# Optimization experiments

Hardware: AMD Instinct MI355X
Metric: run time of the kernel (lower is better)

Reference implementation:

```python
import jax, jax.numpy as jnp
import numpy as np

B, S, F, H, E = 32, 2048, 16, 64, 256

def setup_inputs() -> dict:
    key = jax.random.key(0)
    ks = jax.random.split(key, 7)
    x = jax.random.normal(ks[0], (B, S, F), dtype=jnp.float32)
    masked_index = jax.random.randint(ks[1], (B, S, F), 0, 2) > 0
    W1 = jax.random.normal(ks[2], (F, H), dtype=jnp.float32) * 0.1
    b1 = jax.random.normal(ks[3], (F, H), dtype=jnp.float32) * 0.1
    W2 = jax.random.normal(ks[4], (F, E, H), dtype=jnp.float32) * 0.1
    b2 = jax.random.normal(ks[5], (F, E), dtype=jnp.float32) * 0.1
    masked_values = jax.random.normal(ks[6], (F, E), dtype=jnp.float32)
    return {"x": x, "masked_index": masked_index, "W1": W1, "b1": b1,
            "W2": W2, "b2": b2, "masked_values": masked_values}

def reference(x, masked_index, W1, b1, W2, b2, masked_values):
    # Per-feature 1->64 linear: x[...,None] * W1[f] + b1[f]  -> [B,S,F,H]
    h = jax.nn.gelu(x[..., None] * W1 + b1, approximate=False)
    # dropout is identity in eval mode
    # Per-feature 64->E linear (batched over F): [B,S,F,E]
    embeds = jnp.einsum('bsfh,feh->bsfe', h, W2) + b2
    # Replace masked positions with learned masked_values, then sum over features
    embeds = jnp.where(masked_index[..., None], masked_values, embeds)
    return jnp.sum(embeds, axis=-2)  # [B,S,E]
```

## Files before the change

### kernel.cpp

```cpp
#include <hip/hip_runtime.h>
#include <hip/hip_bf16.h>
#include <cstdint>
#include <math.h>


#define F_ 16
#define H_ 64
#define E_ 256
#define BM 128
#define NT 512
#define BS_TOTAL 65536
#define XSCALE 6.0f

typedef __attribute__((ext_vector_type(8))) short s16x8;
typedef __attribute__((ext_vector_type(4))) float f32x4;

__device__ __forceinline__ unsigned short f2bf(float f){
  unsigned u = __builtin_bit_cast(unsigned, f);
  u += 0x7FFFu + ((u >> 16) & 1u);
  return (unsigned short)(u >> 16);
}
__device__ __forceinline__ unsigned cvtpk(float a, float b){
  unsigned r; asm("v_cvt_pk_bf16_f32 %0, %1, %2" : "=v"(r) : "v"(a), "v"(b)); return r;
}

__global__ __launch_bounds__(256)
void prep_cmat(const float* __restrict__ W1, const float* __restrict__ b1,
               const float* __restrict__ W2, const float* __restrict__ b2,
               const float* __restrict__ mv, unsigned short* __restrict__ Cmat){
  const int f = blockIdx.x, t = threadIdx.x;
  __shared__ float hs[16][H_];
  __shared__ float ct[14][16];

  #pragma unroll
  for (int s = 0; s < 4; ++s){
    int idx = t + s * 256;
    int j = idx >> 6, h = idx & 63;
    float xj = XSCALE * cosf(3.14159265358979f * (j + 0.5f) / 16.0f);
    float z = xj * W1[f * H_ + h] + b1[f * H_ + h];
    hs[j][h] = 0.5f * z * (1.0f + erff(z * 0.7071067811865475f));
  }
  if (t < 224){
    int d = t >> 4, j = t & 15;
    ct[d][j] = cosf(3.14159265358979f * (d + 1) * (j + 0.5f) / 16.0f) * 0.125f;
  }
  __syncthreads();

  const int e = t;
  const float4* w2p = (const float4*)(W2 + ((long)f * E_ + e) * H_);
  float b2v = b2[f * E_ + e];
  float ph[16];
  #pragma unroll
  for (int j = 0; j < 16; ++j) ph[j] = b2v;
  #pragma unroll
  for (int hq = 0; hq < 16; ++hq){
    float4 w = w2p[hq];
    #pragma unroll
    for (int j = 0; j < 16; ++j){
      const float4 hv = *(const float4*)&hs[j][hq * 4];
      ph[j] += w.x * hv.x + w.y * hv.y + w.z * hv.z + w.w * hv.w;
    }
  }
  float s0 = 0.f;
  #pragma unroll
  for (int j = 0; j < 16; ++j) s0 += ph[j];
  float c0 = s0 * 0.0625f;

  float vals[16];
  #pragma unroll
  for (int d = 0; d < 14; ++d){
    float c = 0.f;
    #pragma unroll
    for (int j = 0; j < 16; ++j) c += ph[j] * ct[d][j];
    vals[d] = c;
  }
  vals[14] = mv[f * E_ + e] - c0;
  vals[15] = c0;

  const int lane = (f >> 2) * 16 + (e & 15);
  const int eb = e >> 4;
  #pragma unroll
  for (int g = 0; g < 2; ++g){
    int kk = g * 4 + (f & 3);
    unsigned w[4];
    w[0] = (unsigned)f2bf(vals[g*8+0]) | ((unsigned)f2bf(vals[g*8+1]) << 16);
    w[1] = (unsigned)f2bf(vals[g*8+2]) | ((unsigned)f2bf(vals[g*8+3]) << 16);
    w[2] = (unsigned)f2bf(vals[g*8+4]) | ((unsigned)f2bf(vals[g*8+5]) << 16);
    w[3] = (unsigned)f2bf(vals[g*8+6]) | ((unsigned)f2bf(vals[g*8+7]) << 16);
    long byte = ((long)(kk * 16 + eb) * 64 + lane) * 16;
    *(uint4*)((char*)Cmat + byte) = *(uint4*)w;
  }
}

__global__ __launch_bounds__(NT)
void ts_main(const float* __restrict__ x, const int* __restrict__ mask,
             const unsigned short* __restrict__ Cmat, float* __restrict__ out){
  const int tid = threadIdx.x, lane = tid & 63, wid = tid >> 6;
  const int wm = wid >> 2, wn = wid & 3;
  const int rr = lane & 15;
  const int q  = lane >> 4;
  const int rowBase = blockIdx.x * BM;

  int rows[4];
  #pragma unroll
  for (int m = 0; m < 4; ++m) rows[m] = rowBase + wm * 64 + m * 16 + rr;

  float4 x4[4]; int4 mk4[4];
  #pragma unroll
  for (int m = 0; m < 4; ++m){
    x4[m]  = *(const float4*)&x[rows[m] * F_ + q * 4];
    mk4[m] = *(const int4*)&mask[rows[m] * F_ + q * 4];
  }

  const s16x8* C8 = (const s16x8*)Cmat;
  f32x4 acc[4][4] = {};

  #pragma unroll
  for (int c = 0; c < 4; ++c){
    s16x8 blo[4], bhi[4];
    #pragma unroll
    for (int n = 0; n < 4; ++n){
      blo[n] = C8[((c    ) * 16 + wn * 4 + n) * 64 + lane];
      bhi[n] = C8[((c + 4) * 16 + wn * 4 + n) * 64 + lane];
    }
    s16x8 alo[4], ahi[4];
    #pragma unroll
    for (int m = 0; m < 4; ++m){
      float xv = ((const float*)&x4[m])[c];
      int  mkv = ((const int*)&mk4[m])[c];
      float uu = xv * (1.0f / XSCALE);
      uu = fminf(1.0f, fmaxf(-1.0f, uu));
      float t2 = uu + uu;
      float T1 = uu;
      float T2 = fmaf(t2, T1, -1.0f);
      float T3 = fmaf(t2, T2, -T1);
      float T4 = fmaf(t2, T3, -T2);
      float T5 = fmaf(t2, T4, -T3);
      float T6 = fmaf(t2, T5, -T4);
      float T7 = fmaf(t2, T6, -T5);
      float T8 = fmaf(t2, T7, -T6);
      float T9  = fmaf(t2, T8,  -T7);
      float T10 = fmaf(t2, T9,  -T8);
      float T11 = fmaf(t2, T10, -T9);
      float T12 = fmaf(t2, T11, -T10);
      float T13 = fmaf(t2, T12, -T11);
      float T14 = fmaf(t2, T13, -T12);
      unsigned z = mkv ? 0u : 0xFFFFFFFFu;
      float mf = mkv ? 1.0f : 0.0f;
      union { unsigned w[4]; s16x8 v; } pl, ph;
      pl.w[0] = cvtpk(T1, T2) & z;  pl.w[1] = cvtpk(T3, T4) & z;
      pl.w[2] = cvtpk(T5, T6) & z;  pl.w[3] = cvtpk(T7, T8) & z;
      ph.w[0] = cvtpk(T9, T10) & z; ph.w[1] = cvtpk(T11, T12) & z;
      ph.w[2] = cvtpk(T13, T14) & z; ph.w[3] = cvtpk(mf, 1.0f);
      alo[m] = pl.v; ahi[m] = ph.v;
    }
    #pragma unroll
    for (int m = 0; m < 4; ++m)
      #pragma unroll
      for (int n = 0; n < 4; ++n)
        acc[m][n] = __builtin_amdgcn_mfma_f32_16x16x32_bf16(alo[m], blo[n], acc[m][n], 0, 0, 0);
    #pragma unroll
    for (int m = 0; m < 4; ++m)
      #pragma unroll
      for (int n = 0; n < 4; ++n)
        acc[m][n] = __builtin_amdgcn_mfma_f32_16x16x32_bf16(ahi[m], bhi[n], acc[m][n], 0, 0, 0);
  }

  const int rg = lane >> 4;
  #pragma unroll
  for (int m = 0; m < 4; ++m){
    #pragma unroll
    for (int n = 0; n < 4; ++n){
      int e = wn * 64 + n * 16 + rr;
      int r = rowBase + wm * 64 + m * 16 + rg * 4;
      #pragma unroll
      for (int j = 0; j < 4; ++j)
        out[(long)(r + j) * E_ + e] = acc[m][n][j];
    }
  }
}

extern "C" void kernel_launch(void* const* d_in, const int* in_sizes, int n_in,
                              void* d_out, int out_size, void* d_ws, size_t ws_size,
                              hipStream_t stream) {
  const float* x    = (const float*)d_in[0];
  const int*   mask = (const int*)d_in[1];
  const float* W1   = (const float*)d_in[2];
  const float* b1   = (const float*)d_in[3];
  const float* W2   = (const float*)d_in[4];
  const float* b2   = (const float*)d_in[5];
  const float* mv   = (const float*)d_in[6];
  float* out = (float*)d_out;

  unsigned short* Cmat = (unsigned short*)d_ws;

  prep_cmat<<<dim3(F_), dim3(256), 0, stream>>>(W1, b1, W2, b2, mv, Cmat);
  ts_main<<<dim3(BS_TOTAL / BM), dim3(NT), 0, stream>>>(x, mask, Cmat, out);
}
```

Before: 34.28 us.

## Swap MFMA operands for vectorized float4 output stores, shrink blocks to 64 rows

Swaps the A/B operands of the MFMA so each lane holds four consecutive E values of one row, which lets the epilogue write one 16-byte float4 per tile instead of four scalar stores strided by row. Blocks shrink from 512 threads and 128 rows to 256 threads and 64 rows, doubling the grid, and launch bounds now request three blocks per CU. The int4 mask loads are packed into a 16-bit register to lower register pressure. This targets output-write efficiency and occupancy, at the cost of twice as many blocks each reloading the same Cmat fragments.

```diff
diff --git a/kernel.cpp b/kernel.cpp
--- a/kernel.cpp
+++ b/kernel.cpp
@@ -7,8 +7,7 @@
 #define F_ 16
 #define H_ 64
 #define E_ 256
-#define BM 128
-#define NT 512
+#define NT 256
 #define BS_TOTAL 65536
 #define XSCALE 6.0f
 
@@ -92,24 +91,24 @@
   }
 }
 
-__global__ __launch_bounds__(NT)
+__global__ __launch_bounds__(NT, 3)
 void ts_main(const float* __restrict__ x, const int* __restrict__ mask,
              const unsigned short* __restrict__ Cmat, float* __restrict__ out){
-  const int tid = threadIdx.x, lane = tid & 63, wid = tid >> 6;
-  const int wm = wid >> 2, wn = wid & 3;
+  const int tid = threadIdx.x, lane = tid & 63, wn = tid >> 6;
   const int rr = lane & 15;
   const int q  = lane >> 4;
-  const int rowBase = blockIdx.x * BM;
+  const int rowBase = blockIdx.x * 64;
 
-  int rows[4];
-  #pragma unroll
-  for (int m = 0; m < 4; ++m) rows[m] = rowBase + wm * 64 + m * 16 + rr;
-
-  float4 x4[4]; int4 mk4[4];
+  float4 x4[4]; unsigned mbits = 0;
   #pragma unroll
   for (int m = 0; m < 4; ++m){
-    x4[m]  = *(const float4*)&x[rows[m] * F_ + q * 4];
-    mk4[m] = *(const int4*)&mask[rows[m] * F_ + q * 4];
+    int r = rowBase + m * 16 + rr;
+    x4[m] = *(const float4*)&x[r * F_ + q * 4];
+    int4 mk = *(const int4*)&mask[r * F_ + q * 4];
+    mbits |= (mk.x != 0 ? 1u : 0u) << (m * 4 + 0);
+    mbits |= (mk.y != 0 ? 1u : 0u) << (m * 4 + 1);
+    mbits |= (mk.z != 0 ? 1u : 0u) << (m * 4 + 2);
+    mbits |= (mk.w != 0 ? 1u : 0u) << (m * 4 + 3);
   }
 
   const s16x8* C8 = (const s16x8*)Cmat;
@@ -127,7 +126,7 @@
     #pragma unroll
     for (int m = 0; m < 4; ++m){
       float xv = ((const float*)&x4[m])[c];
-      int  mkv = ((const int*)&mk4[m])[c];
+      unsigned masked = (mbits >> (m * 4 + c)) & 1u;
       float uu = xv * (1.0f / XSCALE);
       uu = fminf(1.0f, fmaxf(-1.0f, uu));
       float t2 = uu + uu;
@@ -145,8 +144,8 @@
       float T12 = fmaf(t2, T11, -T10);
       float T13 = fmaf(t2, T12, -T11);
       float T14 = fmaf(t2, T13, -T12);
-      unsigned z = mkv ? 0u : 0xFFFFFFFFu;
-      float mf = mkv ? 1.0f : 0.0f;
+      unsigned z = masked ? 0u : 0xFFFFFFFFu;
+      float mf = masked ? 1.0f : 0.0f;
       union { unsigned w[4]; s16x8 v; } pl, ph;
       pl.w[0] = cvtpk(T1, T2) & z;  pl.w[1] = cvtpk(T3, T4) & z;
       pl.w[2] = cvtpk(T5, T6) & z;  pl.w[3] = cvtpk(T7, T8) & z;
@@ -158,24 +157,21 @@
     for (int m = 0; m < 4; ++m)
       #pragma unroll
       for (int n = 0; n < 4; ++n)
-        acc[m][n] = __builtin_amdgcn_mfma_f32_16x16x32_bf16(alo[m], blo[n], acc[m][n], 0, 0, 0);
+        acc[m][n] = __builtin_amdgcn_mfma_f32_16x16x32_bf16(blo[n], alo[m], acc[m][n], 0, 0, 0);
     #pragma unroll
     for (int m = 0; m < 4; ++m)
       #pragma unroll
       for (int n = 0; n < 4; ++n)
-        acc[m][n] = __builtin_amdgcn_mfma_f32_16x16x32_bf16(ahi[m], bhi[n], acc[m][n], 0, 0, 0);
+        acc[m][n] = __builtin_amdgcn_mfma_f32_16x16x32_bf16(bhi[n], ahi[m], acc[m][n], 0, 0, 0);
   }
 
-  const int rg = lane >> 4;
   #pragma unroll
   for (int m = 0; m < 4; ++m){
+    int r = rowBase + m * 16 + (lane & 15);
     #pragma unroll
     for (int n = 0; n < 4; ++n){
-      int e = wn * 64 + n * 16 + rr;
-      int r = rowBase + wm * 64 + m * 16 + rg * 4;
-      #pragma unroll
-      for (int j = 0; j < 4; ++j)
-        out[(long)(r + j) * E_ + e] = acc[m][n][j];
+      int e = wn * 64 + n * 16 + (lane >> 4) * 4;
+      *(f32x4*)&out[(long)r * E_ + e] = acc[m][n];
     }
   }
 }
@@ -195,5 +191,5 @@
   unsigned short* Cmat = (unsigned short*)d_ws;
 
   prep_cmat<<<dim3(F_), dim3(256), 0, stream>>>(W1, b1, W2, b2, mv, Cmat);
-  ts_main<<<dim3(BS_TOTAL / BM), dim3(NT), 0, stream>>>(x, mask, Cmat, out);
+  ts_main<<<dim3(BS_TOTAL / 64), dim3(NT), 0, stream>>>(x, mask, Cmat, out);
 }
```

New measurement: 35.22 us. +2.7%, slower.
